# Kernel optimization log

Measured on AMD Instinct MI355X. Metric: run time of the kernel, lower is better.

## Reference

```python
import jax, jax.numpy as jnp
import numpy as np

B, C, L = 2048, 32000, 8
GAMMA = 0.2
BIG = 1e8  # matches torch's 100000000.0 sentinels


def setup_inputs() -> dict:
    key = jax.random.key(0)
    k1, k2, k3 = jax.random.split(key, 3)
    x = jax.random.normal(k1, (B, C), dtype=jnp.float32)
    y = jax.random.randint(k2, (B, L), 0, C, dtype=jnp.int32)
    drop = jax.random.uniform(k3, (B, L)) < 0.3
    drop = drop.at[:, 0].set(False)
    y = jnp.where(drop, -1, y)
    return {"x": x, "y": y}


def reference(x, y):
    b, c = x.shape
    y = y.astype(jnp.int32)
    t = y[:, 0]            # [B] primary targets
    r = y[:, 1:]           # [B, L-1] relative labels, -1 = pad

    # loss1: standard CE(x, t), mean over batch
    logZ = jax.nn.logsumexp(x, axis=1)                       # [B]
    loss1 = jnp.mean(logZ - jnp.take_along_axis(x, t[:, None], axis=1)[:, 0])

    neg_mask = r == -1                                       # [B, L-1]
    sample_mask = jnp.any(~neg_mask, axis=1)                 # [B] rows with >=1 relative

    # min over valid relative logits (argmin+gather in torch == masked min)
    r_safe = jnp.where(neg_mask, 0, r)
    pos_data = jnp.take_along_axis(x, r_safe, axis=1)        # [B, L-1]
    mask_pos_data = jnp.where(neg_mask, BIG, pos_data)
    min_relative = jnp.min(mask_pos_data, axis=1)            # [B]

    # flag: True where class is NOT any of the row's valid labels (incl. target)
    rows = jnp.arange(b, dtype=jnp.int32)[:, None]           # [B,1]
    y_safe = jnp.where(y == -1, 0, y)
    valid = (y != -1).astype(x.dtype)
    mark = jnp.zeros((b, c), x.dtype).at[rows, y_safe].add(valid)
    flag = mark == 0                                         # [B, C]

    new_data = jnp.where(flag, x, -BIG)                      # [B, C]

    # CE over concat([min_relative, new_data], 1) with target 0, per row
    lse = jnp.logaddexp(min_relative, jax.nn.logsumexp(new_data, axis=1))
    loss_row = lse - min_relative                            # [B]

    cnt = jnp.sum(sample_mask.astype(x.dtype))
    loss2 = jnp.sum(jnp.where(sample_mask, loss_row, 0.0)) / jnp.maximum(cnt, 1.0)

    return loss1 + GAMMA * loss2
```

## Files before the change

kernel.cpp:

```cpp
#include <hip/hip_runtime.h>
#include <math.h>

#define B_ROWS 2048
#define C_COLS 32000
#define L_LABELS 8
#define GAMMA_W 0.2f
#define BIG_V 100000000.0f

#define TPB1 320
#define F4T 5
#define CPR 5
#define NBLK1 (B_ROWS * CPR)

__global__ __launch_bounds__(TPB1) void
rll_k1_sum(const float* __restrict__ x, float* __restrict__ part) {
    const int blk = blockIdx.x;
    const int row = blk / CPR;
    const int chunk = blk - row * CPR;
    const int tid = threadIdx.x;
    const float4* __restrict__ x4 =
        reinterpret_cast<const float4*>(x + (size_t)row * C_COLS) + chunk * (TPB1 * F4T);

    float4 buf[F4T];
    #pragma unroll
    for (int k = 0; k < F4T; ++k) buf[k] = x4[tid + k * TPB1];

    float s0 = 0.f, s1 = 0.f, s2 = 0.f, s3 = 0.f;
    #pragma unroll
    for (int k = 0; k < F4T; ++k) {
        s0 += __expf(buf[k].x);
        s1 += __expf(buf[k].y);
        s2 += __expf(buf[k].z);
        s3 += __expf(buf[k].w);
    }
    float s = (s0 + s1) + (s2 + s3);

    #pragma unroll
    for (int off = 32; off > 0; off >>= 1) s += __shfl_xor(s, off, 64);

    __shared__ float ss[TPB1 / 64];
    if ((tid & 63) == 0) ss[tid >> 6] = s;
    __syncthreads();

    if (tid == 0) {
        float t = ss[0];
        #pragma unroll
        for (int w = 1; w < TPB1 / 64; ++w) t += ss[w];
        part[blk] = t;
    }
}

__global__ __launch_bounds__(256) void
rll_k2_row(const float* __restrict__ x, const int* __restrict__ y,
           const float* __restrict__ part, float* __restrict__ prow) {
    const int row = blockIdx.x * 256 + threadIdx.x;

    float s = 0.f;
    #pragma unroll
    for (int c = 0; c < CPR; ++c) s += part[row * CPR + c];
    const float logZ = logf(s);

    const float* __restrict__ xr = x + (size_t)row * C_COLS;
    const int* __restrict__ yr = y + row * L_LABELS;
    int idx[L_LABELS];
    #pragma unroll
    for (int i = 0; i < L_LABELS; ++i) idx[i] = yr[i];

    float xv[L_LABELS];
    xv[0] = xr[idx[0]];
    float minrel = BIG_V;
    bool any_rel = false;
    #pragma unroll
    for (int i = 1; i < L_LABELS; ++i) {
        if (idx[i] >= 0) {
            float v = xr[idx[i]];
            xv[i] = v;
            minrel = fminf(minrel, v);
            any_rel = true;
        }
    }

    const float loss1_contrib = logZ - xv[0];

    float contrib2 = 0.f, cnt = 0.f;
    if (any_rel) {
        float sub = 0.f;
        #pragma unroll
        for (int i = 0; i < L_LABELS; ++i) {
            const bool vi = (i == 0) || (idx[i] >= 0);
            if (!vi) continue;
            bool dup = false;
            #pragma unroll
            for (int j = 0; j < i; ++j) {
                const bool vj = (j == 0) || (idx[j] >= 0);
                if (vj && idx[j] == idx[i]) dup = true;
            }
            if (!dup) sub += expf(xv[i]);
        }
        float s_new = fmaxf(s - sub, 1e-30f);
        const float lse_new = logf(s_new);

        const float a = minrel, b = lse_new;
        const float mx = fmaxf(a, b);
        contrib2 = (mx + log1pf(expf(-fabsf(a - b)))) - a;
        cnt = 1.f;
    }

    prow[row] = loss1_contrib;
    prow[B_ROWS + row] = contrib2;
    prow[2 * B_ROWS + row] = cnt;
}

__global__ __launch_bounds__(1024) void
rll_k3_reduce(const float* __restrict__ p, float* __restrict__ out) {
    const int tid = threadIdx.x;
    float a = p[tid] + p[tid + 1024];
    float b = p[2048 + tid] + p[3072 + tid];
    float c = p[4096 + tid] + p[5120 + tid];

    #pragma unroll
    for (int off = 32; off > 0; off >>= 1) {
        a += __shfl_xor(a, off, 64);
        b += __shfl_xor(b, off, 64);
        c += __shfl_xor(c, off, 64);
    }

    __shared__ float sa[16], sb[16], sc[16];
    const int wave = tid >> 6;
    if ((tid & 63) == 0) { sa[wave] = a; sb[wave] = b; sc[wave] = c; }
    __syncthreads();

    if (tid == 0) {
        float ta = 0.f, tb = 0.f, tc = 0.f;
        #pragma unroll
        for (int w = 0; w < 16; ++w) { ta += sa[w]; tb += sb[w]; tc += sc[w]; }
        const float loss1 = ta / (float)B_ROWS;
        const float loss2 = tb / fmaxf(tc, 1.0f);
        out[0] = loss1 + GAMMA_W * loss2;
    }
}

extern "C" void kernel_launch(void* const* d_in, const int* in_sizes, int n_in,
                              void* d_out, int out_size, void* d_ws, size_t ws_size,
                              hipStream_t stream) {
    const float* x = (const float*)d_in[0];
    const int* yy = (const int*)d_in[1];
    float* out = (float*)d_out;
    float* part = (float*)d_ws;
    float* prow = part + NBLK1;

    rll_k1_sum<<<NBLK1, TPB1, 0, stream>>>(x, part);
    rll_k2_row<<<B_ROWS / 256, 256, 0, stream>>>(x, yy, part, prow);
    rll_k3_reduce<<<1, 1024, 0, stream>>>(prow, out);
}
```

Before: 356.1 us.

## Make sum kernel persistent per-wave with double-buffered register prefetch

Replaces one block per row-chunk with 1280 blocks whose waves each process 8 consecutive 1280-float chunks. The next chunk's loads are issued before the exp-sum of the current one, double-buffering in registers. The block-level shared-memory reduction is removed; each wave writes its own partial, and the row kernel now sums 25 partials per row. This is meant to cut block launch overhead and hide memory latency, at the cost of more registers per thread.

```diff
diff --git a/kernel.cpp b/kernel.cpp
--- a/kernel.cpp
+++ b/kernel.cpp
@@ -7,57 +7,61 @@
 #define GAMMA_W 0.2f
 #define BIG_V 100000000.0f
 
-#define TPB1 320
-#define F4T 5
-#define CPR 5
-#define NBLK1 (B_ROWS * CPR)
+#define TPB 320
+#define NBLK 1280
+#define WAVES_TOT (NBLK * (TPB / 64))
+#define ITERS 8
+#define CHUNK_F4 320
 
-__global__ __launch_bounds__(TPB1) void
-rll_k1_sum(const float* __restrict__ x, float* __restrict__ part) {
-    const int blk = blockIdx.x;
-    const int row = blk / CPR;
-    const int chunk = blk - row * CPR;
-    const int tid = threadIdx.x;
-    const float4* __restrict__ x4 =
-        reinterpret_cast<const float4*>(x + (size_t)row * C_COLS) + chunk * (TPB1 * F4T);
+__global__ __launch_bounds__(TPB, 7) void
+rll_k1_sum(const float* __restrict__ x, float* __restrict__ wpart) {
+    const int lane = threadIdx.x & 63;
+    const int wslot = blockIdx.x * (TPB / 64) + (threadIdx.x >> 6);
+    const int base_ch = wslot * ITERS;
+    const float4* __restrict__ x4 = reinterpret_cast<const float4*>(x);
 
-    float4 buf[F4T];
-    #pragma unroll
-    for (int k = 0; k < F4T; ++k) buf[k] = x4[tid + k * TPB1];
+    float4 A[5], Bv[5];
 
-    float s0 = 0.f, s1 = 0.f, s2 = 0.f, s3 = 0.f;
-    #pragma unroll
-    for (int k = 0; k < F4T; ++k) {
-        s0 += __expf(buf[k].x);
-        s1 += __expf(buf[k].y);
-        s2 += __expf(buf[k].z);
-        s3 += __expf(buf[k].w);
+    {
+        const size_t b = (size_t)base_ch * CHUNK_F4 + lane;
+        #pragma unroll
+        for (int k = 0; k < 5; ++k) A[k] = x4[b + (size_t)k * 64];
     }
-    float s = (s0 + s1) + (s2 + s3);
 
     #pragma unroll
-    for (int off = 32; off > 0; off >>= 1) s += __shfl_xor(s, off, 64);
-
-    __shared__ float ss[TPB1 / 64];
-    if ((tid & 63) == 0) ss[tid >> 6] = s;
-    __syncthreads();
-
-    if (tid == 0) {
-        float t = ss[0];
+    for (int i = 0; i < ITERS; ++i) {
+        if (i + 1 < ITERS) {
+            const size_t b = (size_t)(base_ch + i + 1) * CHUNK_F4 + lane;
+            #pragma unroll
+            for (int k = 0; k < 5; ++k) {
+                if (i & 1) A[k] = x4[b + (size_t)k * 64];
+                else       Bv[k] = x4[b + (size_t)k * 64];
+            }
+        }
+        float s0 = 0.f, s1 = 0.f, s2 = 0.f, s3 = 0.f;
         #pragma unroll
-        for (int w = 1; w < TPB1 / 64; ++w) t += ss[w];
-        part[blk] = t;
+        for (int k = 0; k < 5; ++k) {
+            const float4 v = (i & 1) ? Bv[k] : A[k];
+            s0 += __expf(v.x);
+            s1 += __expf(v.y);
+            s2 += __expf(v.z);
+            s3 += __expf(v.w);
+        }
+        float s = (s0 + s1) + (s2 + s3);
+        #pragma unroll
+        for (int off = 32; off > 0; off >>= 1) s += __shfl_xor(s, off, 64);
+        if (lane == 0) wpart[base_ch + i] = s;
     }
 }
 
 __global__ __launch_bounds__(256) void
 rll_k2_row(const float* __restrict__ x, const int* __restrict__ y,
-           const float* __restrict__ part, float* __restrict__ prow) {
+           const float* __restrict__ wpart, float* __restrict__ prow) {
     const int row = blockIdx.x * 256 + threadIdx.x;
 
     float s = 0.f;
     #pragma unroll
-    for (int c = 0; c < CPR; ++c) s += part[row * CPR + c];
+    for (int c = 0; c < 25; ++c) s += wpart[row * 25 + c];
     const float logZ = logf(s);
 
     const float* __restrict__ xr = x + (size_t)row * C_COLS;
@@ -146,10 +150,10 @@
     const float* x = (const float*)d_in[0];
     const int* yy = (const int*)d_in[1];
     float* out = (float*)d_out;
-    float* part = (float*)d_ws;
-    float* prow = part + NBLK1;
+    float* wpart = (float*)d_ws;
+    float* prow = wpart + (WAVES_TOT * ITERS);
 
-    rll_k1_sum<<<NBLK1, TPB1, 0, stream>>>(x, part);
-    rll_k2_row<<<B_ROWS / 256, 256, 0, stream>>>(x, yy, part, prow);
+    rll_k1_sum<<<NBLK, TPB, 0, stream>>>(x, wpart);
+    rll_k2_row<<<B_ROWS / 256, 256, 0, stream>>>(x, yy, wpart, prow);
     rll_k3_reduce<<<1, 1024, 0, stream>>>(prow, out);
 }
```

New measurement: 359.1 us. About the same (+0.9%).
